# Kernel tuning notes

Hardware: AMD Instinct MI355X
Metric: run time of the kernel (lower is better)

Reference implementation:

```python
import jax, jax.numpy as jnp
import numpy as np

N_NODES = 50000
N_GRAPHS = 512


def _gcn_layer(x, src, dst, W, b):
    # DGL GraphConv, norm='both', allow_zero_in_degree=True
    n = x.shape[0]
    ones = jnp.ones(src.shape[0], x.dtype)
    deg_out = jnp.zeros(n, x.dtype).at[src].add(ones)
    deg_in = jnp.zeros(n, x.dtype).at[dst].add(ones)
    norm_out = jax.lax.rsqrt(jnp.maximum(deg_out, 1.0))
    norm_in = jax.lax.rsqrt(jnp.maximum(deg_in, 1.0))
    h = x * norm_out[:, None]
    agg = jax.ops.segment_sum(h[src], dst, num_segments=n)  # SpMM
    return (agg * norm_in[:, None]) @ W + b


def setup_inputs() -> dict:
    key = jax.random.key(0)
    ks = jax.random.split(key, 16)
    E = 800000
    inp = {
        'nid': jax.random.randint(ks[0], (N_NODES,), 0, 100000),
        'z': jax.random.randint(ks[1], (N_NODES,), 0, 1000),
        'src': jax.random.randint(ks[2], (E,), 0, N_NODES),
        'dst': jax.random.randint(ks[3], (E,), 0, N_NODES),
        'graph_id': jnp.sort(jax.random.randint(ks[4], (N_NODES,), 0, N_GRAPHS)),
        'init_embed': jax.random.normal(ks[5], (100000, 64), jnp.float32) * 0.1,
        'z_table': jax.random.normal(ks[6], (1000, 64), jnp.float32) * 0.1,
        'W0': jax.random.normal(ks[7], (128, 128), jnp.float32) * 0.1,
        'b0': jnp.zeros((128,), jnp.float32),
        'W1': jax.random.normal(ks[8], (128, 128), jnp.float32) * 0.1,
        'b1': jnp.zeros((128,), jnp.float32),
        'W2': jax.random.normal(ks[9], (128, 128), jnp.float32) * 0.1,
        'b2': jnp.zeros((128,), jnp.float32),
        'lin1_W': jax.random.normal(ks[10], (128, 128), jnp.float32) * 0.1,
        'lin1_b': jnp.zeros((128,), jnp.float32),
        'lin2_W': jax.random.normal(ks[11], (128, 200), jnp.float32) * 0.1,
        'lin2_b': jnp.zeros((200,), jnp.float32),
    }
    return inp


def reference(nid, z, src, dst, graph_id, init_embed, z_table, W0, b0, W1, b1, W2, b2, lin1_W, lin1_b, lin2_W, lin2_b):
    # node features: entity embedding lookup + structural label embedding, concat
    x = jnp.concatenate([init_embed[nid], z_table[z]], axis=1)  # [N, 128]
    # layers[:-1] with relu (dropout is identity in eval mode)
    x = jax.nn.relu(_gcn_layer(x, src, dst, W0, b0))
    x = jax.nn.relu(_gcn_layer(x, src, dst, W1, b1))
    x = _gcn_layer(x, src, dst, W2, b2)
    # SumPooling over subgraphs in the batch
    g = jax.ops.segment_sum(x, graph_id, num_segments=N_GRAPHS)  # [G, 128]
    h = jax.nn.relu(g @ lin1_W + lin1_b)
    return h @ lin2_W + lin2_b  # [G, num_rel]
```

## Files before the change

kernel.cpp:

```cpp
#include <hip/hip_runtime.h>
#include <hip/hip_bf16.h>


#define FEAT 128
#define NG 512
#define CH 128
#define NPMAX 12544
#define LDW 136

typedef __attribute__((ext_vector_type(8))) short bf16x8;
typedef __attribute__((ext_vector_type(4))) float f32x4;

__device__ __forceinline__ float bf2f(unsigned short u) {
    union { unsigned int i; float f; } v; v.i = ((unsigned int)u) << 16; return v.f;
}
__device__ __forceinline__ unsigned short f2bf(float f) {
    unsigned int u = __float_as_uint(f);
    return (unsigned short)((u + 0x7FFFu + ((u >> 16) & 1u)) >> 16);
}
__device__ __forceinline__ float lo16(unsigned u) { return __uint_as_float(u << 16); }
__device__ __forceinline__ float hi16(unsigned u) { return __uint_as_float(u & 0xFFFF0000u); }

__global__ __launch_bounds__(256) void k_hist(
        const int* __restrict__ src, const int* __restrict__ dst,
        unsigned* __restrict__ partial_out, unsigned* __restrict__ partial_in,
        int E, int NP, int Ec) {
    __shared__ unsigned h[NPMAX];
    int tid = threadIdx.x;
    int b = blockIdx.x;
    int c = b & (CH - 1);
    const int* __restrict__ arr = (b < CH) ? src : dst;
    unsigned* __restrict__ outp = ((b < CH) ? partial_out : partial_in) + (size_t)c * NP;
    for (int i = tid; i < NP; i += 256) h[i] = 0;
    __syncthreads();
    int e0 = c * Ec, e1 = min(E, e0 + Ec);
    for (int e = e0 + tid; e < e1; e += 256) {
        int v = arr[e];
        atomicAdd(&h[v >> 2], 1u << ((v & 3) * 8));
    }
    __syncthreads();
    for (int i = tid; i < NP; i += 256) outp[i] = h[i];
}

__global__ __launch_bounds__(256) void k_merge(
        unsigned* __restrict__ partial_out, unsigned* __restrict__ partial_in,
        int* __restrict__ cnt_in, float* __restrict__ norm_out,
        float* __restrict__ norm_in, int N, int NP) {
    __shared__ unsigned tile[CH][33];
    __shared__ unsigned sums[32][9];
    int q0 = blockIdx.x * 32;
    int tid = threadIdx.x;
    int qd = tid & 31, k = tid >> 5;

    for (int idx = tid; idx < 32 * CH; idx += 256) {
        int c = idx >> 5, q = idx & 31;
        unsigned v = 0;
        if (q0 + q < NP) v = partial_in[(size_t)c * NP + q0 + q];
        tile[c][q] = v;
    }
    __syncthreads();
    unsigned loc = 0;
    #pragma unroll
    for (int i = 0; i < 16; i++) loc += tile[k * 16 + i][qd];
    sums[qd][k] = loc;
    __syncthreads();
    if (k == 0) {
        unsigned r = 0;
        #pragma unroll
        for (int j = 0; j < 8; j++) { unsigned v = sums[qd][j]; sums[qd][j] = r; r += v; }
        sums[qd][8] = r;
    }
    __syncthreads();
    unsigned run = sums[qd][k];
    #pragma unroll
    for (int i = 0; i < 16; i++) {
        unsigned v = tile[k * 16 + i][qd];
        tile[k * 16 + i][qd] = run;
        run += v;
    }
    __syncthreads();
    for (int idx = tid; idx < 32 * CH; idx += 256) {
        int c = idx >> 5, q = idx & 31;
        if (q0 + q < NP) partial_in[(size_t)c * NP + q0 + q] = tile[c][q];
    }
    __syncthreads();

    for (int idx = tid; idx < 32 * CH; idx += 256) {
        int c = idx >> 5, q = idx & 31;
        unsigned v = 0;
        if (q0 + q < NP) v = partial_out[(size_t)c * NP + q0 + q];
        tile[c][q] = v;
    }
    __syncthreads();
    unsigned loco = 0;
    #pragma unroll
    for (int i = 0; i < 16; i++) loco += tile[k * 16 + i][qd];
    sums[qd][k] = loco;
    __syncthreads();
    if (k == 0) {
        unsigned tot = 0;
        #pragma unroll
        for (int j = 0; j < 8; j++) tot += sums[qd][j];
        unsigned rin = sums[qd][8];
        int w = q0 + qd;
        if (w < NP) {
            #pragma unroll
            for (int j = 0; j < 4; j++) {
                int node = w * 4 + j;
                if (node < N) {
                    unsigned di = (rin >> (j * 8)) & 255u;
                    unsigned dd = (tot >> (j * 8)) & 255u;
                    cnt_in[node]   = (int)di;
                    norm_in[node]  = rsqrtf(fmaxf((float)di, 1.0f));
                    norm_out[node] = rsqrtf(fmaxf((float)dd, 1.0f));
                }
            }
        }
    }
}

__global__ void k_scan_local(const int* __restrict__ cnt, int* __restrict__ excl,
                             int* __restrict__ bsum, int N) {
    __shared__ int s[256];
    int x = threadIdx.x;
    int i = blockIdx.x * 256 + x;
    int v = (i < N) ? cnt[i] : 0;
    s[x] = v;
    __syncthreads();
    for (int off = 1; off < 256; off <<= 1) {
        int t = (x >= off) ? s[x - off] : 0;
        __syncthreads();
        s[x] += t;
        __syncthreads();
    }
    if (i < N) excl[i] = s[x] - v;
    if (x == 255) bsum[blockIdx.x] = s[255];
}

__global__ void k_scan_bsum_prep(int* __restrict__ bsum, int* __restrict__ boff, int nb,
                                 const float* __restrict__ W0, const float* __restrict__ W1,
                                 unsigned short* __restrict__ WF0, unsigned short* __restrict__ WF1) {
    if (blockIdx.x == 0) {
        __shared__ int s[256];
        int x = threadIdx.x;
        int v = (x < nb) ? bsum[x] : 0;
        s[x] = v;
        __syncthreads();
        for (int off = 1; off < 256; off <<= 1) {
            int t = (x >= off) ? s[x - off] : 0;
            __syncthreads();
            s[x] += t;
            __syncthreads();
        }
        if (x < nb) boff[x] = s[x] - v;
    } else {
        int t = ((int)blockIdx.x - 1) * 256 + threadIdx.x;
        const float* __restrict__ W = (t < 16384) ? W0 : W1;
        unsigned short* __restrict__ WF = (t < 16384) ? WF0 : WF1;
        int tt = t & 16383;
        int f = tt >> 9, l = (tt >> 3) & 63, e = tt & 7;
        int n = (f >> 2) * 16 + (l & 15);
        int k = (f & 3) * 32 + (l >> 4) * 8 + e;
        WF[tt] = f2bf(W[k * 128 + n]);
    }
}

__global__ void k_add_off(int* __restrict__ row_start, const int* __restrict__ boff,
                          float* __restrict__ g, int N) {
    int i = blockIdx.x * blockDim.x + threadIdx.x;
    int stride = gridDim.x * blockDim.x;
    if (i < N) row_start[i] += boff[i >> 8];
    for (int j = i; j < NG * FEAT; j += stride) g[j] = 0.f;
}

__global__ __launch_bounds__(256) void k_fill_bx(
        const int* __restrict__ src, const int* __restrict__ dst,
        const int* __restrict__ row_start, const unsigned* __restrict__ partial_in,
        unsigned short* __restrict__ csr,
        const int* __restrict__ nid, const int* __restrict__ z,
        const float* __restrict__ emb, const float* __restrict__ zt,
        const float* __restrict__ nout, unsigned short* __restrict__ x,
        int N, int E, int NP, int Ec) {
    if ((int)blockIdx.x < CH) {
        __shared__ unsigned cur[NPMAX];
        int tid = threadIdx.x;
        int c = blockIdx.x;
        const unsigned* __restrict__ pre = partial_in + (size_t)c * NP;
        for (int i = tid; i < NP; i += 256) cur[i] = pre[i];
        __syncthreads();
        int e0 = c * Ec, e1 = min(E, e0 + Ec);
        for (int e = e0 + tid; e < e1; e += 256) {
            int d = dst[e], s = src[e];
            int sh = (d & 3) * 8;
            unsigned t = atomicAdd(&cur[d >> 2], 1u << sh);
            int off = (int)((t >> sh) & 255u);
            csr[row_start[d] + off] = (unsigned short)s;
        }
    } else {
        int tid = ((int)blockIdx.x - CH) * 256 + threadIdx.x;
        int i = tid >> 5, q = tid & 31;
        if (i < N) {
            float4 v;
            if (q < 16) v = ((const float4*)emb)[(size_t)nid[i] * 16 + q];
            else        v = ((const float4*)zt)[(size_t)z[i] * 16 + (q - 16)];
            float w = nout[i];
            ushort4 u;
            u.x = f2bf(v.x * w); u.y = f2bf(v.y * w);
            u.z = f2bf(v.z * w); u.w = f2bf(v.w * w);
            ((ushort4*)x)[(size_t)i * 32 + q] = u;
        }
    }
}

#define ACC8(u)                                                                  \
    a0 += lo16(u.x); a1 += hi16(u.x); a2 += lo16(u.y); a3 += hi16(u.y);          \
    a4 += lo16(u.z); a5 += hi16(u.z); a6 += lo16(u.w); a7 += hi16(u.w);

#define GATHER_LOOP                                                              \
    {                                                                            \
        int base = row_start[node];                                              \
        int n = cnt_in[node];                                                    \
        const uint4* xp = (const uint4*)x;                   \
        for (int j0 = 0; j0 < n; j0 += 16) {                                     \
            int rem = n - j0;                                                    \
            int m = rem < 16 ? rem : 16;                                         \
            int e = (int)csr[base + j0 + (ql < m ? ql : 0)];                     \
            int j = 0;                                                           \
            for (; j + 8 <= m; j += 8) {                                         \
                int s0 = __shfl(e, j + 0, 16), s1 = __shfl(e, j + 1, 16);        \
                int s2 = __shfl(e, j + 2, 16), s3 = __shfl(e, j + 3, 16);        \
                int s4 = __shfl(e, j + 4, 16), s5 = __shfl(e, j + 5, 16);        \
                int s6 = __shfl(e, j + 6, 16), s7 = __shfl(e, j + 7, 16);        \
                uint4 u0 = xp[(size_t)s0 * 16 + ql];                             \
                uint4 u1 = xp[(size_t)s1 * 16 + ql];                             \
                uint4 u2 = xp[(size_t)s2 * 16 + ql];                             \
                uint4 u3 = xp[(size_t)s3 * 16 + ql];                             \
                uint4 u4 = xp[(size_t)s4 * 16 + ql];                             \
                uint4 u5 = xp[(size_t)s5 * 16 + ql];                             \
                uint4 u6 = xp[(size_t)s6 * 16 + ql];                             \
                uint4 u7 = xp[(size_t)s7 * 16 + ql];                             \
                ACC8(u0) ACC8(u1) ACC8(u2) ACC8(u3)                              \
                ACC8(u4) ACC8(u5) ACC8(u6) ACC8(u7)                              \
            }                                                                    \
            for (; j + 4 <= m; j += 4) {                                         \
                int s0 = __shfl(e, j + 0, 16), s1 = __shfl(e, j + 1, 16);        \
                int s2 = __shfl(e, j + 2, 16), s3 = __shfl(e, j + 3, 16);        \
                uint4 u0 = xp[(size_t)s0 * 16 + ql];                             \
                uint4 u1 = xp[(size_t)s1 * 16 + ql];                             \
                uint4 u2 = xp[(size_t)s2 * 16 + ql];                             \
                uint4 u3 = xp[(size_t)s3 * 16 + ql];                             \
                ACC8(u0) ACC8(u1) ACC8(u2) ACC8(u3)                              \
            }                                                                    \
            for (; j < m; j++) {                                                 \
                int s = __shfl(e, j, 16);                                        \
                uint4 u = xp[(size_t)s * 16 + ql];                               \
                ACC8(u)                                                          \
            }                                                                    \
        }                                                                        \
    }

__global__ __launch_bounds__(256, 8) void k_gather_gemm(
        const unsigned short* __restrict__ x, const float* __restrict__ nin,
        const unsigned short* __restrict__ csr, const int* __restrict__ row_start,
        const int* __restrict__ cnt_in, const unsigned short* __restrict__ WF,
        const float* __restrict__ bias, const float* __restrict__ nout,
        unsigned short* __restrict__ y, int N) {
    __shared__ unsigned short As[16 * LDW];
    int tid = threadIdx.x;
    int nb = blockIdx.x * 16;
    int ql = tid & 15;
    int nl = tid >> 4;
    int node = nb + nl;

    float a0 = 0.f, a1 = 0.f, a2 = 0.f, a3 = 0.f;
    float a4 = 0.f, a5 = 0.f, a6 = 0.f, a7 = 0.f;
    if (node < N) {
        GATHER_LOOP
        float ni = nin[node];
        a0 *= ni; a1 *= ni; a2 *= ni; a3 *= ni;
        a4 *= ni; a5 *= ni; a6 *= ni; a7 *= ni;
    }
    uint4 o;
    o.x = (unsigned)f2bf(a0) | ((unsigned)f2bf(a1) << 16);
    o.y = (unsigned)f2bf(a2) | ((unsigned)f2bf(a3) << 16);
    o.z = (unsigned)f2bf(a4) | ((unsigned)f2bf(a5) << 16);
    o.w = (unsigned)f2bf(a6) | ((unsigned)f2bf(a7) << 16);
    *(uint4*)(As + nl * LDW + ql * 8) = o;
    __syncthreads();

    int lane = tid & 63;
    int wv = tid >> 6;
    int c = lane & 15, q = lane >> 4;

    const unsigned short* ap = As + c * LDW + q * 8;
    bf16x8 fa0 = *(const bf16x8*)(ap);
    bf16x8 fa1 = *(const bf16x8*)(ap + 32);
    bf16x8 fa2 = *(const bf16x8*)(ap + 64);
    bf16x8 fa3 = *(const bf16x8*)(ap + 96);
    const bf16x8* __restrict__ wf = (const bf16x8*)WF;
    __syncthreads();

    #pragma unroll
    for (int t = 0; t < 2; t++) {
        int nt = wv * 2 + t;
        bf16x8 fb0 = wf[(nt * 4 + 0) * 64 + lane];
        bf16x8 fb1 = wf[(nt * 4 + 1) * 64 + lane];
        bf16x8 fb2 = wf[(nt * 4 + 2) * 64 + lane];
        bf16x8 fb3 = wf[(nt * 4 + 3) * 64 + lane];
        float bb = bias[nt * 16 + c];
        f32x4 acc = {bb, bb, bb, bb};
        acc = __builtin_amdgcn_mfma_f32_16x16x32_bf16(fa0, fb0, acc, 0, 0, 0);
        acc = __builtin_amdgcn_mfma_f32_16x16x32_bf16(fa1, fb1, acc, 0, 0, 0);
        acc = __builtin_amdgcn_mfma_f32_16x16x32_bf16(fa2, fb2, acc, 0, 0, 0);
        acc = __builtin_amdgcn_mfma_f32_16x16x32_bf16(fa3, fb3, acc, 0, 0, 0);
        #pragma unroll
        for (int rr = 0; rr < 4; rr++) {
            int row = q * 4 + rr;
            float s = nout[min(nb + row, N - 1)];
            As[row * LDW + nt * 16 + c] = f2bf(fmaxf(acc[rr], 0.f) * s);
        }
    }
    __syncthreads();

    {
        int row = tid >> 4, seg = tid & 15;
        int nd = nb + row;
        if (nd < N) {
            const ushort4* p = (const ushort4*)(As + row * LDW + seg * 8);
            ushort4* d = (ushort4*)(y + (size_t)nd * 128 + seg * 8);
            d[0] = p[0]; d[1] = p[1];
        }
    }
}

__global__ __launch_bounds__(256, 8) void k_gather_pool(
        const unsigned short* __restrict__ x, const float* __restrict__ nin,
        const unsigned short* __restrict__ csr, const int* __restrict__ row_start,
        const int* __restrict__ cnt_in, const int* __restrict__ gid,
        float* __restrict__ g, int N) {
    __shared__ __align__(16) float gl[16][132];
    __shared__ int slots[16];
    int tid = threadIdx.x;
    int nb = blockIdx.x * 16;
    int ql = tid & 15;
    int nl = tid >> 4;
    int node = nb + nl;

    float a0 = 0.f, a1 = 0.f, a2 = 0.f, a3 = 0.f;
    float a4 = 0.f, a5 = 0.f, a6 = 0.f, a7 = 0.f;
    int slot = -1;
    if (node < N) {
        GATHER_LOOP
        float ni = nin[node];
        a0 *= ni; a1 *= ni; a2 *= ni; a3 *= ni;
        a4 *= ni; a5 *= ni; a6 *= ni; a7 *= ni;
        slot = gid[node];
    }
    float4* row = (float4*)&gl[nl][ql * 8];
    row[0] = make_float4(a0, a1, a2, a3);
    row[1] = make_float4(a4, a5, a6, a7);
    if (ql == 0) slots[nl] = slot;
    __syncthreads();

    int h = tid >> 7;
    int j = tid & 127;
    int prev = -1;
    float acc = 0.f;
    #pragma unroll
    for (int i = h * 8; i < h * 8 + 8; i++) {
        int s = slots[i];
        if (s != prev) {
            if (prev >= 0) atomicAdd(&g[(size_t)prev * FEAT + j], acc);
            acc = 0.f;
            prev = s;
        }
        acc += gl[i][j];
    }
    if (prev >= 0) atomicAdd(&g[(size_t)prev * FEAT + j], acc);
}

__global__ __launch_bounds__(256) void k_head(
        const float* __restrict__ g, const int* __restrict__ gid,
        const float* __restrict__ W2, const float* __restrict__ b2,
        const float* __restrict__ l1W, const float* __restrict__ l1b,
        const float* __restrict__ l2W, const float* __restrict__ l2b,
        float* __restrict__ out, int N) {
    __shared__ float gs[128];
    __shared__ float ys[128];
    __shared__ float hs[128];
    int gi = blockIdx.x, tid = threadIdx.x;

    int lo = 0, hi = N;
    while (lo < hi) { int m = (lo + hi) >> 1; if (gid[m] < gi) lo = m + 1; else hi = m; }
    int s0 = lo;
    lo = 0; hi = N;
    while (lo < hi) { int m = (lo + hi) >> 1; if (gid[m] < gi + 1) lo = m + 1; else hi = m; }
    float cnt = (float)(lo - s0);

    if (tid < 128) gs[tid] = g[(size_t)gi * FEAT + tid];
    __syncthreads();
    if (tid < 128) {
        float a = cnt * b2[tid];
        for (int k = 0; k < 128; k++) a += gs[k] * W2[(size_t)k * 128 + tid];
        ys[tid] = a;
    }
    __syncthreads();
    if (tid < 128) {
        float a = l1b[tid];
        for (int k = 0; k < 128; k++) a += ys[k] * l1W[(size_t)k * 128 + tid];
        hs[tid] = fmaxf(a, 0.f);
    }
    __syncthreads();
    if (tid < 200) {
        float a = l2b[tid];
        for (int k = 0; k < 128; k++) a += hs[k] * l2W[(size_t)k * 200 + tid];
        out[(size_t)gi * 200 + tid] = a;
    }
}

extern "C" void kernel_launch(void* const* d_in, const int* in_sizes, int n_in,
                              void* d_out, int out_size, void* d_ws, size_t ws_size,
                              hipStream_t stream) {
    const int*   nid = (const int*)d_in[0];
    const int*   z   = (const int*)d_in[1];
    const int*   src = (const int*)d_in[2];
    const int*   dst = (const int*)d_in[3];
    const int*   gid = (const int*)d_in[4];
    const float* emb = (const float*)d_in[5];
    const float* zt  = (const float*)d_in[6];
    const float* W0  = (const float*)d_in[7];
    const float* b0  = (const float*)d_in[8];
    const float* W1  = (const float*)d_in[9];
    const float* b1  = (const float*)d_in[10];
    const float* W2  = (const float*)d_in[11];
    const float* b2  = (const float*)d_in[12];
    const float* l1W = (const float*)d_in[13];
    const float* l1b = (const float*)d_in[14];
    const float* l2W = (const float*)d_in[15];
    const float* l2b = (const float*)d_in[16];
    float* out = (float*)d_out;

    const int N = in_sizes[0];
    const int E = in_sizes[2];
    const int NB = (N + 255) / 256;
    const int NP = (N + 3) / 4;
    const int Ec = (E + CH - 1) / CH;

    size_t NA = (size_t)((N + 63) & ~63);
    float* norm_out = (float*)d_ws;
    float* norm_in  = norm_out + NA;
    float* g        = norm_in + NA;
    unsigned short* xA  = (unsigned short*)(g + (size_t)NG * FEAT);
    unsigned short* xB  = xA + (size_t)N * FEAT;
    unsigned short* WF0 = xB + (size_t)N * FEAT;
    unsigned short* WF1 = WF0 + 128 * 128;
    int* cnt_in    = (int*)(WF1 + 128 * 128);
    int* row_start = cnt_in + NA;
    int* bsum      = row_start + NA;
    int* boff      = bsum + 256;
    unsigned* partial_out = (unsigned*)(boff + 256);
    unsigned* partial_in  = partial_out + (size_t)CH * NP;
    unsigned short* csr = (unsigned short*)(partial_in + (size_t)CH * NP);

    k_hist<<<2 * CH, 256, 0, stream>>>(src, dst, partial_out, partial_in, E, NP, Ec);
    k_merge<<<(NP + 31) / 32, 256, 0, stream>>>(partial_out, partial_in, cnt_in,
                                                norm_out, norm_in, N, NP);
    k_scan_local<<<NB, 256, 0, stream>>>(cnt_in, row_start, bsum, N);
    k_scan_bsum_prep<<<1 + 128, 256, 0, stream>>>(bsum, boff, NB, W0, W1, WF0, WF1);
    k_add_off<<<NB, 256, 0, stream>>>(row_start, boff, g, N);
    int XB = (N * 32 + 255) / 256;
    k_fill_bx<<<CH + XB, 256, 0, stream>>>(src, dst, row_start, partial_in, csr,
                                           nid, z, emb, zt, norm_out, xA, N, E, NP, Ec);

    int gg_blocks = (N + 15) / 16;

    k_gather_gemm<<<gg_blocks, 256, 0, stream>>>(xA, norm_in, csr, row_start, cnt_in,
                                                 WF0, b0, norm_out, xB, N);
    k_gather_gemm<<<gg_blocks, 256, 0, stream>>>(xB, norm_in, csr, row_start, cnt_in,
                                                 WF1, b1, norm_out, xA, N);
    k_gather_pool<<<gg_blocks, 256, 0, stream>>>(xA, norm_in, csr, row_start, cnt_in,
                                                 gid, g, N);

    k_head<<<NG, 256, 0, stream>>>(g, gid, W2, b2, l1W, l1b, l2W, l2b, out, N);
}
```

Measured before the change: 276.3 us.

## Chunk feature layout and pad CSR rows for branch-free 16-wide gathers

Node features are now stored as four column-chunks of 32 bf16 each, with a zero sentinel row at index N. Each CSR row is padded to a multiple of 16 and the padding points at the sentinel, so the gather loop reads neighbor indices as uint4 vectors and issues 16 unrolled 4-byte loads per chunk with no remainder handling. The histogram/fill chunk count doubles, and the fused fill/build-x kernel is split into two kernels. The padding adds CSR memory and extra fill work, each gather becomes four passes over the neighbor list with narrower loads, and the occupancy hint is removed.

```diff
diff --git a/kernel.cpp b/kernel.cpp
--- a/kernel.cpp
+++ b/kernel.cpp
@@ -4,16 +4,14 @@
 
 #define FEAT 128
 #define NG 512
-#define CH 128
+#define CH 256
+#define SEG (CH / 8)
 #define NPMAX 12544
 #define LDW 136
 
 typedef __attribute__((ext_vector_type(8))) short bf16x8;
 typedef __attribute__((ext_vector_type(4))) float f32x4;
 
-__device__ __forceinline__ float bf2f(unsigned short u) {
-    union { unsigned int i; float f; } v; v.i = ((unsigned int)u) << 16; return v.f;
-}
 __device__ __forceinline__ unsigned short f2bf(float f) {
     unsigned int u = __float_as_uint(f);
     return (unsigned short)((u + 0x7FFFu + ((u >> 16) & 1u)) >> 16);
@@ -61,7 +59,7 @@
     __syncthreads();
     unsigned loc = 0;
     #pragma unroll
-    for (int i = 0; i < 16; i++) loc += tile[k * 16 + i][qd];
+    for (int i = 0; i < SEG; i++) loc += tile[k * SEG + i][qd];
     sums[qd][k] = loc;
     __syncthreads();
     if (k == 0) {
@@ -73,9 +71,9 @@
     __syncthreads();
     unsigned run = sums[qd][k];
     #pragma unroll
-    for (int i = 0; i < 16; i++) {
-        unsigned v = tile[k * 16 + i][qd];
-        tile[k * 16 + i][qd] = run;
+    for (int i = 0; i < SEG; i++) {
+        unsigned v = tile[k * SEG + i][qd];
+        tile[k * SEG + i][qd] = run;
         run += v;
     }
     __syncthreads();
@@ -94,7 +92,7 @@
     __syncthreads();
     unsigned loco = 0;
     #pragma unroll
-    for (int i = 0; i < 16; i++) loco += tile[k * 16 + i][qd];
+    for (int i = 0; i < SEG; i++) loco += tile[k * SEG + i][qd];
     sums[qd][k] = loco;
     __syncthreads();
     if (k == 0) {
@@ -124,7 +122,7 @@
     __shared__ int s[256];
     int x = threadIdx.x;
     int i = blockIdx.x * 256 + x;
-    int v = (i < N) ? cnt[i] : 0;
+    int v = (i < N) ? ((cnt[i] + 15) & ~15) : 0;
     s[x] = v;
     __syncthreads();
     for (int off = 1; off < 256; off <<= 1) {
@@ -166,100 +164,104 @@
 }
 
 __global__ void k_add_off(int* __restrict__ row_start, const int* __restrict__ boff,
-                          float* __restrict__ g, int N) {
+                          float* __restrict__ g, unsigned short* __restrict__ csr,
+                          unsigned short* __restrict__ xA, unsigned short* __restrict__ xB,
+                          int N, int csrtot) {
     int i = blockIdx.x * blockDim.x + threadIdx.x;
     int stride = gridDim.x * blockDim.x;
+    size_t CSU = (size_t)(N + 1) * 32;
     if (i < N) row_start[i] += boff[i >> 8];
     for (int j = i; j < NG * FEAT; j += stride) g[j] = 0.f;
-}
-
-__global__ __launch_bounds__(256) void k_fill_bx(
+    for (int j = i; j < csrtot; j += stride) csr[j] = (unsigned short)N;
+    for (int j = i; j < 256; j += stride) {
+        unsigned short* xp = (j < 128) ? xA : xB;
+        int c = (j >> 5) & 3, kk = j & 31;
+        xp[(size_t)c * CSU + (size_t)N * 32 + kk] = 0;
+    }
+}
+
+__global__ __launch_bounds__(256) void k_fill(
         const int* __restrict__ src, const int* __restrict__ dst,
         const int* __restrict__ row_start, const unsigned* __restrict__ partial_in,
-        unsigned short* __restrict__ csr,
+        unsigned short* __restrict__ csr, int N, int E, int NP, int Ec) {
+    __shared__ unsigned cur[NPMAX];
+    int tid = threadIdx.x;
+    int c = blockIdx.x;
+    const unsigned* __restrict__ pre = partial_in + (size_t)c * NP;
+    for (int i = tid; i < NP; i += 256) cur[i] = pre[i];
+    __syncthreads();
+    int e0 = c * Ec, e1 = min(E, e0 + Ec);
+    for (int e = e0 + tid; e < e1; e += 256) {
+        int d = dst[e], s = src[e];
+        int sh = (d & 3) * 8;
+        unsigned t = atomicAdd(&cur[d >> 2], 1u << sh);
+        int off = (int)((t >> sh) & 255u);
+        csr[row_start[d] + off] = (unsigned short)s;
+    }
+}
+
+__global__ __launch_bounds__(256) void k_build_x(
         const int* __restrict__ nid, const int* __restrict__ z,
         const float* __restrict__ emb, const float* __restrict__ zt,
-        const float* __restrict__ nout, unsigned short* __restrict__ x,
-        int N, int E, int NP, int Ec) {
-    if ((int)blockIdx.x < CH) {
-        __shared__ unsigned cur[NPMAX];
-        int tid = threadIdx.x;
-        int c = blockIdx.x;
-        const unsigned* __restrict__ pre = partial_in + (size_t)c * NP;
-        for (int i = tid; i < NP; i += 256) cur[i] = pre[i];
-        __syncthreads();
-        int e0 = c * Ec, e1 = min(E, e0 + Ec);
-        for (int e = e0 + tid; e < e1; e += 256) {
-            int d = dst[e], s = src[e];
-            int sh = (d & 3) * 8;
-            unsigned t = atomicAdd(&cur[d >> 2], 1u << sh);
-            int off = (int)((t >> sh) & 255u);
-            csr[row_start[d] + off] = (unsigned short)s;
-        }
-    } else {
-        int tid = ((int)blockIdx.x - CH) * 256 + threadIdx.x;
-        int i = tid >> 5, q = tid & 31;
-        if (i < N) {
-            float4 v;
-            if (q < 16) v = ((const float4*)emb)[(size_t)nid[i] * 16 + q];
-            else        v = ((const float4*)zt)[(size_t)z[i] * 16 + (q - 16)];
-            float w = nout[i];
-            ushort4 u;
-            u.x = f2bf(v.x * w); u.y = f2bf(v.y * w);
-            u.z = f2bf(v.z * w); u.w = f2bf(v.w * w);
-            ((ushort4*)x)[(size_t)i * 32 + q] = u;
-        }
-    }
-}
-
-#define ACC8(u)                                                                  \
-    a0 += lo16(u.x); a1 += hi16(u.x); a2 += lo16(u.y); a3 += hi16(u.y);          \
-    a4 += lo16(u.z); a5 += hi16(u.z); a6 += lo16(u.w); a7 += hi16(u.w);
-
-#define GATHER_LOOP                                                              \
+        const float* __restrict__ nout, unsigned short* __restrict__ x, int N) {
+    int t = blockIdx.x * 256 + threadIdx.x;
+    int i = t >> 5, q = t & 31;
+    if (i >= N) return;
+    size_t CSU = (size_t)(N + 1) * 32;
+    float4 v;
+    if (q < 16) v = ((const float4*)emb)[(size_t)nid[i] * 16 + q];
+    else        v = ((const float4*)zt)[(size_t)z[i] * 16 + (q - 16)];
+    float w = nout[i];
+    ushort4 u;
+    u.x = f2bf(v.x * w); u.y = f2bf(v.y * w);
+    u.z = f2bf(v.z * w); u.w = f2bf(v.w * w);
+    int cch = q >> 3;
+    int wi = (q * 4) & 31;
+    *(ushort4*)(x + (size_t)cch * CSU + (size_t)i * 32 + wi) = u;
+}
+
+#define ACCU(u, A0, A1) A0 += lo16(u); A1 += hi16(u);
+#define GATHER_CHUNK(P, A0, A1)                                                  \
     {                                                                            \
-        int base = row_start[node];                                              \
-        int n = cnt_in[node];                                                    \
-        const uint4* xp = (const uint4*)x;                   \
+        const unsigned* __restrict__ xq = xch + (size_t)(P) * CS2;               \
         for (int j0 = 0; j0 < n; j0 += 16) {                                     \
-            int rem = n - j0;                                                    \
-            int m = rem < 16 ? rem : 16;                                         \
-            int e = (int)csr[base + j0 + (ql < m ? ql : 0)];                     \
-            int j = 0;                                                           \
-            for (; j + 8 <= m; j += 8) {                                         \
-                int s0 = __shfl(e, j + 0, 16), s1 = __shfl(e, j + 1, 16);        \
-                int s2 = __shfl(e, j + 2, 16), s3 = __shfl(e, j + 3, 16);        \
-                int s4 = __shfl(e, j + 4, 16), s5 = __shfl(e, j + 5, 16);        \
-                int s6 = __shfl(e, j + 6, 16), s7 = __shfl(e, j + 7, 16);        \
-                uint4 u0 = xp[(size_t)s0 * 16 + ql];                             \
-                uint4 u1 = xp[(size_t)s1 * 16 + ql];                             \
-                uint4 u2 = xp[(size_t)s2 * 16 + ql];                             \
-                uint4 u3 = xp[(size_t)s3 * 16 + ql];                             \
-                uint4 u4 = xp[(size_t)s4 * 16 + ql];                             \
-                uint4 u5 = xp[(size_t)s5 * 16 + ql];                             \
-                uint4 u6 = xp[(size_t)s6 * 16 + ql];                             \
-                uint4 u7 = xp[(size_t)s7 * 16 + ql];                             \
-                ACC8(u0) ACC8(u1) ACC8(u2) ACC8(u3)                              \
-                ACC8(u4) ACC8(u5) ACC8(u6) ACC8(u7)                              \
-            }                                                                    \
-            for (; j + 4 <= m; j += 4) {                                         \
-                int s0 = __shfl(e, j + 0, 16), s1 = __shfl(e, j + 1, 16);        \
-                int s2 = __shfl(e, j + 2, 16), s3 = __shfl(e, j + 3, 16);        \
-                uint4 u0 = xp[(size_t)s0 * 16 + ql];                             \
-                uint4 u1 = xp[(size_t)s1 * 16 + ql];                             \
-                uint4 u2 = xp[(size_t)s2 * 16 + ql];                             \
-                uint4 u3 = xp[(size_t)s3 * 16 + ql];                             \
-                ACC8(u0) ACC8(u1) ACC8(u2) ACC8(u3)                              \
-            }                                                                    \
-            for (; j < m; j++) {                                                 \
-                int s = __shfl(e, j, 16);                                        \
-                uint4 u = xp[(size_t)s * 16 + ql];                               \
-                ACC8(u)                                                          \
-            }                                                                    \
+            uint4 qa = cp[(j0 >> 3)];                                            \
+            uint4 qb = cp[(j0 >> 3) + 1];                                        \
+            unsigned u0  = xq[(qa.x & 0xFFFFu) * 16];                            \
+            unsigned u1  = xq[(qa.x >> 16) * 16];                                \
+            unsigned u2  = xq[(qa.y & 0xFFFFu) * 16];                            \
+            unsigned u3  = xq[(qa.y >> 16) * 16];                                \
+            unsigned u4  = xq[(qa.z & 0xFFFFu) * 16];                            \
+            unsigned u5  = xq[(qa.z >> 16) * 16];                                \
+            unsigned u6  = xq[(qa.w & 0xFFFFu) * 16];                            \
+            unsigned u7  = xq[(qa.w >> 16) * 16];                                \
+            unsigned u8  = xq[(qb.x & 0xFFFFu) * 16];                            \
+            unsigned u9  = xq[(qb.x >> 16) * 16];                                \
+            unsigned u10 = xq[(qb.y & 0xFFFFu) * 16];                            \
+            unsigned u11 = xq[(qb.y >> 16) * 16];                                \
+            unsigned u12 = xq[(qb.z & 0xFFFFu) * 16];                            \
+            unsigned u13 = xq[(qb.z >> 16) * 16];                                \
+            unsigned u14 = xq[(qb.w & 0xFFFFu) * 16];                            \
+            unsigned u15 = xq[(qb.w >> 16) * 16];                                \
+            ACCU(u0, A0, A1)  ACCU(u1, A0, A1)  ACCU(u2, A0, A1)  ACCU(u3, A0, A1)   \
+            ACCU(u4, A0, A1)  ACCU(u5, A0, A1)  ACCU(u6, A0, A1)  ACCU(u7, A0, A1)   \
+            ACCU(u8, A0, A1)  ACCU(u9, A0, A1)  ACCU(u10, A0, A1) ACCU(u11, A0, A1)  \
+            ACCU(u12, A0, A1) ACCU(u13, A0, A1) ACCU(u14, A0, A1) ACCU(u15, A0, A1)  \
         }                                                                        \
     }
 
-__global__ __launch_bounds__(256, 8) void k_gather_gemm(
+#define GATHER_ALL                                                               \
+    int base = row_start[node];                                                  \
+    int n = cnt_in[node];                                                        \
+    const uint4* __restrict__ cp = (const uint4*)(csr + base);                   \
+    const unsigned* __restrict__ xch = (const unsigned*)x + ql;                  \
+    const size_t CS2 = (size_t)(N + 1) * 16;                                     \
+    GATHER_CHUNK(0, c0a, c0b)                                                    \
+    GATHER_CHUNK(1, c1a, c1b)                                                    \
+    GATHER_CHUNK(2, c2a, c2b)                                                    \
+    GATHER_CHUNK(3, c3a, c3b)
+
+__global__ __launch_bounds__(256) void k_gather_gemm(
         const unsigned short* __restrict__ x, const float* __restrict__ nin,
         const unsigned short* __restrict__ csr, const int* __restrict__ row_start,
         const int* __restrict__ cnt_in, const unsigned short* __restrict__ WF,
@@ -272,20 +274,19 @@
     int nl = tid >> 4;
     int node = nb + nl;
 
-    float a0 = 0.f, a1 = 0.f, a2 = 0.f, a3 = 0.f;
-    float a4 = 0.f, a5 = 0.f, a6 = 0.f, a7 = 0.f;
+    float c0a = 0.f, c0b = 0.f, c1a = 0.f, c1b = 0.f;
+    float c2a = 0.f, c2b = 0.f, c3a = 0.f, c3b = 0.f;
     if (node < N) {
-        GATHER_LOOP
+        GATHER_ALL
         float ni = nin[node];
-        a0 *= ni; a1 *= ni; a2 *= ni; a3 *= ni;
-        a4 *= ni; a5 *= ni; a6 *= ni; a7 *= ni;
-    }
-    uint4 o;
-    o.x = (unsigned)f2bf(a0) | ((unsigned)f2bf(a1) << 16);
-    o.y = (unsigned)f2bf(a2) | ((unsigned)f2bf(a3) << 16);
-    o.z = (unsigned)f2bf(a4) | ((unsigned)f2bf(a5) << 16);
-    o.w = (unsigned)f2bf(a6) | ((unsigned)f2bf(a7) << 16);
-    *(uint4*)(As + nl * LDW + ql * 8) = o;
+        c0a *= ni; c0b *= ni; c1a *= ni; c1b *= ni;
+        c2a *= ni; c2b *= ni; c3a *= ni; c3b *= ni;
+    }
+    unsigned short* ar = As + nl * LDW + ql * 2;
+    *(unsigned*)(ar +  0) = (unsigned)f2bf(c0a) | ((unsigned)f2bf(c0b) << 16);
+    *(unsigned*)(ar + 32) = (unsigned)f2bf(c1a) | ((unsigned)f2bf(c1b) << 16);
+    *(unsigned*)(ar + 64) = (unsigned)f2bf(c2a) | ((unsigned)f2bf(c2b) << 16);
+    *(unsigned*)(ar + 96) = (unsigned)f2bf(c3a) | ((unsigned)f2bf(c3b) << 16);
     __syncthreads();
 
     int lane = tid & 63;
@@ -323,17 +324,19 @@
     __syncthreads();
 
     {
+        size_t CSU = (size_t)(N + 1) * 32;
         int row = tid >> 4, seg = tid & 15;
         int nd = nb + row;
         if (nd < N) {
+            int cch = seg >> 2, wi = (seg & 3) * 8;
             const ushort4* p = (const ushort4*)(As + row * LDW + seg * 8);
-            ushort4* d = (ushort4*)(y + (size_t)nd * 128 + seg * 8);
+            ushort4* d = (ushort4*)(y + (size_t)cch * CSU + (size_t)nd * 32 + wi);
             d[0] = p[0]; d[1] = p[1];
         }
     }
 }
 
-__global__ __launch_bounds__(256, 8) void k_gather_pool(
+__global__ __launch_bounds__(256) void k_gather_pool(
         const unsigned short* __restrict__ x, const float* __restrict__ nin,
         const unsigned short* __restrict__ csr, const int* __restrict__ row_start,
         const int* __restrict__ cnt_in, const int* __restrict__ gid,
@@ -346,19 +349,23 @@
     int nl = tid >> 4;
     int node = nb + nl;
 
-    float a0 = 0.f, a1 = 0.f, a2 = 0.f, a3 = 0.f;
-    float a4 = 0.f, a5 = 0.f, a6 = 0.f, a7 = 0.f;
+    float c0a = 0.f, c0b = 0.f, c1a = 0.f, c1b = 0.f;
+    float c2a = 0.f, c2b = 0.f, c3a = 0.f, c3b = 0.f;
     int slot = -1;
     if (node < N) {
-        GATHER_LOOP
+        GATHER_ALL
         float ni = nin[node];
-        a0 *= ni; a1 *= ni; a2 *= ni; a3 *= ni;
-        a4 *= ni; a5 *= ni; a6 *= ni; a7 *= ni;
+        c0a *= ni; c0b *= ni; c1a *= ni; c1b *= ni;
+        c2a *= ni; c2b *= ni; c3a *= ni; c3b *= ni;
         slot = gid[node];
     }
-    float4* row = (float4*)&gl[nl][ql * 8];
-    row[0] = make_float4(a0, a1, a2, a3);
-    row[1] = make_float4(a4, a5, a6, a7);
+    {
+        float2* r0 = (float2*)&gl[nl][ql * 2];
+        r0[0]  = make_float2(c0a, c0b);
+        *(float2*)&gl[nl][32 + ql * 2] = make_float2(c1a, c1b);
+        *(float2*)&gl[nl][64 + ql * 2] = make_float2(c2a, c2b);
+        *(float2*)&gl[nl][96 + ql * 2] = make_float2(c3a, c3b);
+    }
     if (ql == 0) slots[nl] = slot;
     __syncthreads();
 
@@ -445,14 +452,16 @@
     const int NB = (N + 255) / 256;
     const int NP = (N + 3) / 4;
     const int Ec = (E + CH - 1) / CH;
+    const int CSRTOT = E + 16 * N + 64;
+    const size_t XSZ = (size_t)4 * (N + 1) * 32;
 
     size_t NA = (size_t)((N + 63) & ~63);
     float* norm_out = (float*)d_ws;
     float* norm_in  = norm_out + NA;
     float* g        = norm_in + NA;
     unsigned short* xA  = (unsigned short*)(g + (size_t)NG * FEAT);
-    unsigned short* xB  = xA + (size_t)N * FEAT;
-    unsigned short* WF0 = xB + (size_t)N * FEAT;
+    unsigned short* xB  = xA + XSZ;
+    unsigned short* WF0 = xB + XSZ;
     unsigned short* WF1 = WF0 + 128 * 128;
     int* cnt_in    = (int*)(WF1 + 128 * 128);
     int* row_start = cnt_in + NA;
@@ -467,10 +476,9 @@
                                                 norm_out, norm_in, N, NP);
     k_scan_local<<<NB, 256, 0, stream>>>(cnt_in, row_start, bsum, N);
     k_scan_bsum_prep<<<1 + 128, 256, 0, stream>>>(bsum, boff, NB, W0, W1, WF0, WF1);
-    k_add_off<<<NB, 256, 0, stream>>>(row_start, boff, g, N);
-    int XB = (N * 32 + 255) / 256;
-    k_fill_bx<<<CH + XB, 256, 0, stream>>>(src, dst, row_start, partial_in, csr,
-                                           nid, z, emb, zt, norm_out, xA, N, E, NP, Ec);
+    k_add_off<<<NB, 256, 0, stream>>>(row_start, boff, g, csr, xA, xB, N, CSRTOT);
+    k_build_x<<<(N * 32 + 255) / 256, 256, 0, stream>>>(nid, z, emb, zt, norm_out, xA, N);
+    k_fill<<<CH, 256, 0, stream>>>(src, dst, row_start, partial_in, csr, N, E, NP, Ec);
 
     int gg_blocks = (N + 15) / 16;
 
```

Result: slower. 303.3 us (+9.8%).

## Fuse embedding gather into merge, drop add-offset kernel, fold g-zeroing into prep

Applied to the files above, without the earlier changes.

Moves the input embedding lookup and norm_out scaling into k_merge, so each block writes x for the 128 nodes whose degrees it just computed, using a shared-memory copy of norm_out. Removes k_add_off: block offsets are added on the fly (excl + boff) in the CSR fill and in the gather loops, and zeroing of g moves into extra blocks of the prep kernel. This cuts two kernel launches and one pass over row_start, at the cost of an extra boff load per node in the gather kernels and a heavier k_merge.

```diff
diff --git a/kernel.cpp b/kernel.cpp
--- a/kernel.cpp
+++ b/kernel.cpp
@@ -5,15 +5,13 @@
 #define FEAT 128
 #define NG 512
 #define CH 128
+#define SEG (CH / 8)
 #define NPMAX 12544
 #define LDW 136
 
 typedef __attribute__((ext_vector_type(8))) short bf16x8;
 typedef __attribute__((ext_vector_type(4))) float f32x4;
 
-__device__ __forceinline__ float bf2f(unsigned short u) {
-    union { unsigned int i; float f; } v; v.i = ((unsigned int)u) << 16; return v.f;
-}
 __device__ __forceinline__ unsigned short f2bf(float f) {
     unsigned int u = __float_as_uint(f);
     return (unsigned short)((u + 0x7FFFu + ((u >> 16) & 1u)) >> 16);
@@ -45,9 +43,13 @@
 __global__ __launch_bounds__(256) void k_merge(
         unsigned* __restrict__ partial_out, unsigned* __restrict__ partial_in,
         int* __restrict__ cnt_in, float* __restrict__ norm_out,
-        float* __restrict__ norm_in, int N, int NP) {
+        float* __restrict__ norm_in,
+        const int* __restrict__ nid, const int* __restrict__ z,
+        const float* __restrict__ emb, const float* __restrict__ zt,
+        unsigned short* __restrict__ x, int N, int NP) {
     __shared__ unsigned tile[CH][33];
     __shared__ unsigned sums[32][9];
+    __shared__ float nout_l[128];
     int q0 = blockIdx.x * 32;
     int tid = threadIdx.x;
     int qd = tid & 31, k = tid >> 5;
@@ -61,7 +63,7 @@
     __syncthreads();
     unsigned loc = 0;
     #pragma unroll
-    for (int i = 0; i < 16; i++) loc += tile[k * 16 + i][qd];
+    for (int i = 0; i < SEG; i++) loc += tile[k * SEG + i][qd];
     sums[qd][k] = loc;
     __syncthreads();
     if (k == 0) {
@@ -73,9 +75,9 @@
     __syncthreads();
     unsigned run = sums[qd][k];
     #pragma unroll
-    for (int i = 0; i < 16; i++) {
-        unsigned v = tile[k * 16 + i][qd];
-        tile[k * 16 + i][qd] = run;
+    for (int i = 0; i < SEG; i++) {
+        unsigned v = tile[k * SEG + i][qd];
+        tile[k * SEG + i][qd] = run;
         run += v;
     }
     __syncthreads();
@@ -94,7 +96,7 @@
     __syncthreads();
     unsigned loco = 0;
     #pragma unroll
-    for (int i = 0; i < 16; i++) loco += tile[k * 16 + i][qd];
+    for (int i = 0; i < SEG; i++) loco += tile[k * SEG + i][qd];
     sums[qd][k] = loco;
     __syncthreads();
     if (k == 0) {
@@ -112,9 +114,28 @@
                     unsigned dd = (tot >> (j * 8)) & 255u;
                     cnt_in[node]   = (int)di;
                     norm_in[node]  = rsqrtf(fmaxf((float)di, 1.0f));
-                    norm_out[node] = rsqrtf(fmaxf((float)dd, 1.0f));
+                    float no = rsqrtf(fmaxf((float)dd, 1.0f));
+                    norm_out[node] = no;
+                    nout_l[qd * 4 + j] = no;
                 }
             }
+        }
+    }
+    __syncthreads();
+
+    int nbase = q0 * 4;
+    for (int t = tid; t < 128 * 32; t += 256) {
+        int nl = t >> 5, q = t & 31;
+        int node = nbase + nl;
+        if (node < N) {
+            float4 v;
+            if (q < 16) v = ((const float4*)emb)[(size_t)nid[node] * 16 + q];
+            else        v = ((const float4*)zt)[(size_t)z[node] * 16 + (q - 16)];
+            float w = nout_l[nl];
+            ushort4 u;
+            u.x = f2bf(v.x * w); u.y = f2bf(v.y * w);
+            u.z = f2bf(v.z * w); u.w = f2bf(v.w * w);
+            *(ushort4*)(x + (size_t)node * FEAT + q * 4) = u;
         }
     }
 }
@@ -139,7 +160,8 @@
 
 __global__ void k_scan_bsum_prep(int* __restrict__ bsum, int* __restrict__ boff, int nb,
                                  const float* __restrict__ W0, const float* __restrict__ W1,
-                                 unsigned short* __restrict__ WF0, unsigned short* __restrict__ WF1) {
+                                 unsigned short* __restrict__ WF0, unsigned short* __restrict__ WF1,
+                                 float* __restrict__ g) {
     if (blockIdx.x == 0) {
         __shared__ int s[256];
         int x = threadIdx.x;
@@ -153,7 +175,7 @@
             __syncthreads();
         }
         if (x < nb) boff[x] = s[x] - v;
-    } else {
+    } else if ((int)blockIdx.x <= 128) {
         int t = ((int)blockIdx.x - 1) * 256 + threadIdx.x;
         const float* __restrict__ W = (t < 16384) ? W0 : W1;
         unsigned short* __restrict__ WF = (t < 16384) ? WF0 : WF1;
@@ -162,53 +184,31 @@
         int n = (f >> 2) * 16 + (l & 15);
         int k = (f & 3) * 32 + (l >> 4) * 8 + e;
         WF[tt] = f2bf(W[k * 128 + n]);
-    }
-}
-
-__global__ void k_add_off(int* __restrict__ row_start, const int* __restrict__ boff,
-                          float* __restrict__ g, int N) {
-    int i = blockIdx.x * blockDim.x + threadIdx.x;
-    int stride = gridDim.x * blockDim.x;
-    if (i < N) row_start[i] += boff[i >> 8];
-    for (int j = i; j < NG * FEAT; j += stride) g[j] = 0.f;
-}
-
-__global__ __launch_bounds__(256) void k_fill_bx(
+    } else {
+        int j0 = ((int)blockIdx.x - 129) * 2048 + threadIdx.x * 8;
+        #pragma unroll
+        for (int j = 0; j < 8; j++) g[j0 + j] = 0.f;
+    }
+}
+
+__global__ __launch_bounds__(256) void k_fill(
         const int* __restrict__ src, const int* __restrict__ dst,
-        const int* __restrict__ row_start, const unsigned* __restrict__ partial_in,
-        unsigned short* __restrict__ csr,
-        const int* __restrict__ nid, const int* __restrict__ z,
-        const float* __restrict__ emb, const float* __restrict__ zt,
-        const float* __restrict__ nout, unsigned short* __restrict__ x,
-        int N, int E, int NP, int Ec) {
-    if ((int)blockIdx.x < CH) {
-        __shared__ unsigned cur[NPMAX];
-        int tid = threadIdx.x;
-        int c = blockIdx.x;
-        const unsigned* __restrict__ pre = partial_in + (size_t)c * NP;
-        for (int i = tid; i < NP; i += 256) cur[i] = pre[i];
-        __syncthreads();
-        int e0 = c * Ec, e1 = min(E, e0 + Ec);
-        for (int e = e0 + tid; e < e1; e += 256) {
-            int d = dst[e], s = src[e];
-            int sh = (d & 3) * 8;
-            unsigned t = atomicAdd(&cur[d >> 2], 1u << sh);
-            int off = (int)((t >> sh) & 255u);
-            csr[row_start[d] + off] = (unsigned short)s;
-        }
-    } else {
-        int tid = ((int)blockIdx.x - CH) * 256 + threadIdx.x;
-        int i = tid >> 5, q = tid & 31;
-        if (i < N) {
-            float4 v;
-            if (q < 16) v = ((const float4*)emb)[(size_t)nid[i] * 16 + q];
-            else        v = ((const float4*)zt)[(size_t)z[i] * 16 + (q - 16)];
-            float w = nout[i];
-            ushort4 u;
-            u.x = f2bf(v.x * w); u.y = f2bf(v.y * w);
-            u.z = f2bf(v.z * w); u.w = f2bf(v.w * w);
-            ((ushort4*)x)[(size_t)i * 32 + q] = u;
-        }
+        const int* __restrict__ excl, const int* __restrict__ boff,
+        const unsigned* __restrict__ partial_in,
+        unsigned short* __restrict__ csr, int N, int E, int NP, int Ec) {
+    __shared__ unsigned cur[NPMAX];
+    int tid = threadIdx.x;
+    int c = blockIdx.x;
+    const unsigned* __restrict__ pre = partial_in + (size_t)c * NP;
+    for (int i = tid; i < NP; i += 256) cur[i] = pre[i];
+    __syncthreads();
+    int e0 = c * Ec, e1 = min(E, e0 + Ec);
+    for (int e = e0 + tid; e < e1; e += 256) {
+        int d = dst[e], s = src[e];
+        int sh = (d & 3) * 8;
+        unsigned t = atomicAdd(&cur[d >> 2], 1u << sh);
+        int off = (int)((t >> sh) & 255u);
+        csr[excl[d] + boff[d >> 8] + off] = (unsigned short)s;
     }
 }
 
@@ -218,7 +218,7 @@
 
 #define GATHER_LOOP                                                              \
     {                                                                            \
-        int base = row_start[node];                                              \
+        int base = row_start[node] + boff[node >> 8];                            \
         int n = cnt_in[node];                                                    \
         const uint4* xp = (const uint4*)x;                   \
         for (int j0 = 0; j0 < n; j0 += 16) {                                     \
@@ -262,7 +262,8 @@
 __global__ __launch_bounds__(256, 8) void k_gather_gemm(
         const unsigned short* __restrict__ x, const float* __restrict__ nin,
         const unsigned short* __restrict__ csr, const int* __restrict__ row_start,
-        const int* __restrict__ cnt_in, const unsigned short* __restrict__ WF,
+        const int* __restrict__ boff, const int* __restrict__ cnt_in,
+        const unsigned short* __restrict__ WF,
         const float* __restrict__ bias, const float* __restrict__ nout,
         unsigned short* __restrict__ y, int N) {
     __shared__ unsigned short As[16 * LDW];
@@ -327,7 +328,7 @@
         int nd = nb + row;
         if (nd < N) {
             const ushort4* p = (const ushort4*)(As + row * LDW + seg * 8);
-            ushort4* d = (ushort4*)(y + (size_t)nd * 128 + seg * 8);
+            ushort4* d = (ushort4*)(y + (size_t)nd * FEAT + seg * 8);
             d[0] = p[0]; d[1] = p[1];
         }
     }
@@ -336,8 +337,8 @@
 __global__ __launch_bounds__(256, 8) void k_gather_pool(
         const unsigned short* __restrict__ x, const float* __restrict__ nin,
         const unsigned short* __restrict__ csr, const int* __restrict__ row_start,
-        const int* __restrict__ cnt_in, const int* __restrict__ gid,
-        float* __restrict__ g, int N) {
+        const int* __restrict__ boff, const int* __restrict__ cnt_in,
+        const int* __restrict__ gid, float* __restrict__ g, int N) {
     __shared__ __align__(16) float gl[16][132];
     __shared__ int slots[16];
     int tid = threadIdx.x;
@@ -455,8 +456,8 @@
     unsigned short* WF0 = xB + (size_t)N * FEAT;
     unsigned short* WF1 = WF0 + 128 * 128;
     int* cnt_in    = (int*)(WF1 + 128 * 128);
-    int* row_start = cnt_in + NA;
-    int* bsum      = row_start + NA;
+    int* excl      = cnt_in + NA;
+    int* bsum      = excl + NA;
     int* boff      = bsum + 256;
     unsigned* partial_out = (unsigned*)(boff + 256);
     unsigned* partial_in  = partial_out + (size_t)CH * NP;
@@ -464,21 +465,20 @@
 
     k_hist<<<2 * CH, 256, 0, stream>>>(src, dst, partial_out, partial_in, E, NP, Ec);
     k_merge<<<(NP + 31) / 32, 256, 0, stream>>>(partial_out, partial_in, cnt_in,
-                                                norm_out, norm_in, N, NP);
-    k_scan_local<<<NB, 256, 0, stream>>>(cnt_in, row_start, bsum, N);
-    k_scan_bsum_prep<<<1 + 128, 256, 0, stream>>>(bsum, boff, NB, W0, W1, WF0, WF1);
-    k_add_off<<<NB, 256, 0, stream>>>(row_start, boff, g, N);
-    int XB = (N * 32 + 255) / 256;
-    k_fill_bx<<<CH + XB, 256, 0, stream>>>(src, dst, row_start, partial_in, csr,
-                                           nid, z, emb, zt, norm_out, xA, N, E, NP, Ec);
+                                                norm_out, norm_in, nid, z, emb, zt,
+                                                xA, N, NP);
+    k_scan_local<<<NB, 256, 0, stream>>>(cnt_in, excl, bsum, N);
+    k_scan_bsum_prep<<<1 + 128 + 32, 256, 0, stream>>>(bsum, boff, NB, W0, W1,
+                                                       WF0, WF1, g);
+    k_fill<<<CH, 256, 0, stream>>>(src, dst, excl, boff, partial_in, csr, N, E, NP, Ec);
 
     int gg_blocks = (N + 15) / 16;
 
-    k_gather_gemm<<<gg_blocks, 256, 0, stream>>>(xA, norm_in, csr, row_start, cnt_in,
+    k_gather_gemm<<<gg_blocks, 256, 0, stream>>>(xA, norm_in, csr, excl, boff, cnt_in,
                                                  WF0, b0, norm_out, xB, N);
-    k_gather_gemm<<<gg_blocks, 256, 0, stream>>>(xB, norm_in, csr, row_start, cnt_in,
+    k_gather_gemm<<<gg_blocks, 256, 0, stream>>>(xB, norm_in, csr, excl, boff, cnt_in,
                                                  WF1, b1, norm_out, xA, N);
-    k_gather_pool<<<gg_blocks, 256, 0, stream>>>(xA, norm_in, csr, row_start, cnt_in,
+    k_gather_pool<<<gg_blocks, 256, 0, stream>>>(xA, norm_in, csr, excl, boff, cnt_in,
                                                  gid, g, N);
 
     k_head<<<NG, 256, 0, stream>>>(g, gid, W2, b2, l1W, l1b, l2W, l2b, out, N);
```

After: 283.9 us. 1.03x slower.
